# Kernel optimization log

Measured on AMD Instinct MI355X. Metric: run time of the kernel, lower is better.

## Reference

```python
import jax, jax.numpy as jnp
import numpy as np

OUT, IN, G, TOK = 4096, 4096, 16, 8192


def setup_inputs() -> dict:
    key = jax.random.key(0)
    k1, k2, k3, k4 = jax.random.split(key, 4)
    x = jax.random.normal(k1, (TOK, IN), dtype=jnp.float32)
    # packed int4 pairs: each byte holds two 4-bit values (low nibble, high nibble)
    weight_q4 = jax.random.randint(k2, (OUT * IN // G, G // 2), 0, 256, dtype=jnp.int32)
    # per-group abs-max normalization, strictly positive
    weight_norm = jax.random.uniform(k3, (OUT * IN // G, 1), dtype=jnp.float16, minval=0.01, maxval=1.0)
    bias = jax.random.normal(k4, (OUT,), dtype=jnp.float32) * 0.01
    return {"x": x, "weight_q4": weight_q4, "weight_norm": weight_norm, "bias": bias}


def _dequant_4bit(weight_q4, weight_norm):
    # unpack nibbles: even positions = low nibble, odd positions = high nibble
    low = weight_q4 & 15
    high = (weight_q4 >> 4) & 15
    q8 = jnp.stack([low, high], axis=-1).reshape(weight_q4.shape[0], -1)  # [n_groups, G]
    norm = weight_norm.astype(jnp.float32)                                 # [n_groups, 1]
    w = (q8.astype(jnp.float32) / 15.0) * 2.0 * norm - norm               # [-norm, +norm]
    return w.reshape(OUT, IN)


def reference(x, weight_q4, weight_norm, bias):
    W = _dequant_4bit(weight_q4, weight_norm)  # [OUT, IN] fp32
    return x @ W.T + bias                      # [TOK, OUT]
```

## Files before the change

### kernel.cpp

```cpp
#include <hip/hip_runtime.h>
#include <hip/hip_fp16.h>

#define M_TOK 8192
#define N_OUT 4096
#define K_IN  4096
#define GRP   16

typedef __bf16 bf16x8 __attribute__((ext_vector_type(8)));
typedef float  f32x4  __attribute__((ext_vector_type(4)));
typedef unsigned short ushort8 __attribute__((ext_vector_type(8)));

__device__ __forceinline__ float bfbits(unsigned short h) {
    unsigned int u = ((unsigned int)h) << 16;
    return __builtin_bit_cast(float, u);
}

#define GLDS16(gp, sp) __builtin_amdgcn_global_load_lds(                      \
        (const __attribute__((address_space(1))) void*)(gp),                  \
        (__attribute__((address_space(3))) void*)(sp), 16, 0, 0)

__device__ __forceinline__ void detect_block(const void* __restrict__ xv,
                                             const void* __restrict__ nrmv,
                                             const void* __restrict__ biasv,
                                             int* s_modes) {
    const int tid = threadIdx.x;
    if (tid < 64) {
        const unsigned short* px = (const unsigned short*)xv;
        unsigned short hx = px[tid * 2];
        int ex = (hx >> 7) & 0xFF;
        bool xok = ((ex >= 64 && ex <= 134) || (hx & 0x7FFF) == 0);
        unsigned long long xb = __ballot(xok);

        const unsigned short* pn = (const unsigned short*)nrmv;
        unsigned short hn = pn[tid & 31];
        float v16 = __half2float(__builtin_bit_cast(__half, hn));
        float vbf = bfbits(hn);
        unsigned long long b16 = __ballot(v16 > 0.0085f && v16 < 1.02f);
        unsigned long long bbf = __ballot(vbf > 0.0085f && vbf < 1.02f);

        const unsigned short* pb = (const unsigned short*)biasv;
        unsigned short hb = pb[tid * 2];
        int eb = (hb >> 7) & 0xFF;
        bool bok = ((eb >= 64 && eb <= 134) || (hb & 0x7FFF) == 0);
        unsigned long long bb = __ballot(bok);

        if (tid == 0) {
            s_modes[0] = (xb == ~0ULL) ? 1 : 0;
            s_modes[1] = (b16 == ~0ULL) ? 0 : ((bbf == ~0ULL) ? 1 : 2);
            s_modes[2] = (bb == ~0ULL) ? 1 : 0;
        }
    }
    __syncthreads();
}

__global__ __launch_bounds__(256) void prep_all(const void* __restrict__ xv,
                                                const int* __restrict__ q4,
                                                const void* __restrict__ nrmv,
                                                const void* __restrict__ biasv,
                                                __bf16* __restrict__ W,
                                                __bf16* __restrict__ X) {
    __shared__ int s_modes[3];
    detect_block(xv, nrmv, biasv, s_modes);
    const int tid = threadIdx.x;

    if (blockIdx.x < 4096) {
        const int nmode = s_modes[1];
        const int t = blockIdx.x * 256 + tid;
        const int4* qp = (const int4*)q4 + (size_t)t * 2;
        int4 a4 = qp[0], c4 = qp[1];
        float nm;
        if (nmode == 0)      nm = __half2float(((const __half*)nrmv)[t]);
        else if (nmode == 1) nm = bfbits(((const unsigned short*)nrmv)[t]);
        else                 nm = ((const float*)nrmv)[t];
        float s = nm * (2.0f / 15.0f);
        int qs[8] = {a4.x, a4.y, a4.z, a4.w, c4.x, c4.y, c4.z, c4.w};
        bf16x8 v0, v1;
#pragma unroll
        for (int u = 0; u < 8; ++u) {
            float lo = fmaf((float)(qs[u] & 15), s, -nm);
            float hi = fmaf((float)((qs[u] >> 4) & 15), s, -nm);
            if (u < 4) { v0[2 * u] = (__bf16)lo; v0[2 * u + 1] = (__bf16)hi; }
            else       { v1[2 * (u - 4)] = (__bf16)lo; v1[2 * (u - 4) + 1] = (__bf16)hi; }
        }
        bf16x8* wp = (bf16x8*)(W + (size_t)t * 16);
        wp[0] = v0; wp[1] = v1;
    } else {
        if (s_modes[0] == 1) return;
        const int bx = blockIdx.x - 4096;
        const int total8 = M_TOK * K_IN / 8;
        const int stride = 2048 * 256;
        for (int i = bx * 256 + tid; i < total8; i += stride) {
            const float4* fp = (const float4*)xv + (size_t)i * 2;
            float4 f0 = fp[0], f1 = fp[1];
            bf16x8 u;
            u[0] = (__bf16)f0.x; u[1] = (__bf16)f0.y; u[2] = (__bf16)f0.z; u[3] = (__bf16)f0.w;
            u[4] = (__bf16)f1.x; u[5] = (__bf16)f1.y; u[6] = (__bf16)f1.z; u[7] = (__bf16)f1.w;
            *(bf16x8*)(X + (size_t)i * 8) = u;
        }
    }
}

__global__ __launch_bounds__(256, 3) void gemm_glds(
        const void* __restrict__ xv, const __bf16* __restrict__ Xws,
        const __bf16* __restrict__ W, const void* __restrict__ nrmv,
        const void* __restrict__ biasv, float* __restrict__ out) {
    __shared__ __align__(16) __bf16 As[128 * 32];
    __shared__ __align__(16) __bf16 Bs[128 * 32];
    __shared__ int s_modes[3];

    detect_block(xv, nrmv, biasv, s_modes);
    const int xmode = s_modes[0];
    const int bmode = s_modes[2];
    const __bf16* A = xmode ? (const __bf16*)xv : Xws;

    const int bid = ((blockIdx.x & 7) << 8) + (blockIdx.x >> 3);
    const int n0 = (bid & 31) * 128;
    const int m0 = (bid >> 5) * 128;

    const int tid = threadIdx.x;
    const int w  = tid >> 6;
    const int l  = tid & 63;
    const int r  = l & 15;
    const int q  = l >> 4;
    const int wm = (w >> 1) * 64;
    const int wn = (w & 1) * 64;

    const int c0 = w * 2;
    const int lr = l >> 2;
    const int lc = (l & 3) * 8;
    const __bf16* ga0 = A + (size_t)(m0 + c0 * 16 + lr) * K_IN + lc;
    const __bf16* gb0 = W + (size_t)(n0 + c0 * 16 + lr) * K_IN + lc;
    __bf16* la0 = As + c0 * 512;
    __bf16* lb0 = Bs + c0 * 512;

    f32x4 acc[4][4];
#pragma unroll
    for (int j = 0; j < 4; ++j) {
        const int bidx = n0 + wn + j * 16 + r;
        float bv = (bmode == 0) ? ((const float*)biasv)[bidx]
                                : bfbits(((const unsigned short*)biasv)[bidx]);
#pragma unroll
        for (int i = 0; i < 4; ++i) {
            acc[i][j][0] = bv; acc[i][j][1] = bv; acc[i][j][2] = bv; acc[i][j][3] = bv;
        }
    }

    for (int k0 = 0; k0 < K_IN; k0 += 32) {
        __syncthreads();
        GLDS16(ga0 + k0,                      la0);
        GLDS16(ga0 + k0 + (size_t)16 * K_IN,  la0 + 512);
        GLDS16(gb0 + k0,                      lb0);
        GLDS16(gb0 + k0 + (size_t)16 * K_IN,  lb0 + 512);
        __syncthreads();

        bf16x8 af[4], bf[4];
#pragma unroll
        for (int i = 0; i < 4; ++i)
            af[i] = *(const bf16x8*)(As + (wm + i * 16 + r) * 32 + q * 8);
#pragma unroll
        for (int j = 0; j < 4; ++j)
            bf[j] = *(const bf16x8*)(Bs + (wn + j * 16 + r) * 32 + q * 8);

#pragma unroll
        for (int i = 0; i < 4; ++i)
#pragma unroll
            for (int j = 0; j < 4; ++j)
                acc[i][j] = __builtin_amdgcn_mfma_f32_16x16x32_bf16(
                    af[i], bf[j], acc[i][j], 0, 0, 0);
    }

#pragma unroll
    for (int i = 0; i < 4; ++i) {
        const int row = m0 + wm + i * 16 + q * 4;
#pragma unroll
        for (int j = 0; j < 4; ++j) {
            const int col = n0 + wn + j * 16 + r;
            float* p = out + (size_t)row * N_OUT + col;
            p[0 * N_OUT] = acc[i][j][0];
            p[1 * N_OUT] = acc[i][j][1];
            p[2 * N_OUT] = acc[i][j][2];
            p[3 * N_OUT] = acc[i][j][3];
        }
    }
}

__global__ __launch_bounds__(256, 2) void gemm_fused(
        const void* __restrict__ xv,
        const int* __restrict__ q4, const void* __restrict__ nrmv,
        const void* __restrict__ biasv, float* __restrict__ out) {
    __shared__ __align__(16) __bf16 As[128 * 32];
    __shared__ __align__(16) __bf16 Bs[128 * 32];
    __shared__ int s_modes[3];

    detect_block(xv, nrmv, biasv, s_modes);
    const int tid = threadIdx.x;
    const int xmode = s_modes[0];
    const int nmode = s_modes[1];
    const int bmode = s_modes[2];

    const int bid = blockIdx.x;
    const int n0 = (bid & 31) * 128;
    const int m0 = (bid >> 5) * 128;

    const int w  = tid >> 6;
    const int l  = tid & 63;
    const int r  = l & 15;
    const int q  = l >> 4;
    const int wm = (w >> 1) * 64;
    const int wn = (w & 1) * 64;

    const int arow = tid >> 1;
    const int acol = (tid & 1) * 16;
    const size_t aoff = (size_t)(m0 + arow) * K_IN + acol;

    const int brow = tid >> 1;
    const int bgc  = tid & 1;

    f32x4 acc[4][4];
#pragma unroll
    for (int j = 0; j < 4; ++j) {
        const int bidx = n0 + wn + j * 16 + r;
        float bv = (bmode == 0) ? ((const float*)biasv)[bidx]
                                : bfbits(((const unsigned short*)biasv)[bidx]);
#pragma unroll
        for (int i = 0; i < 4; ++i) {
            acc[i][j][0] = bv; acc[i][j][1] = bv; acc[i][j][2] = bv; acc[i][j][3] = bv;
        }
    }

    for (int k0 = 0; k0 < K_IN; k0 += 32) {
        __syncthreads();
        {
            const int g = (n0 + brow) * (K_IN / GRP) + (k0 >> 4) + bgc;
            const int4* qp = (const int4*)q4 + (size_t)g * 2;
            int4 a4 = qp[0], c4 = qp[1];
            float nm;
            if (nmode == 0)      nm = __half2float(((const __half*)nrmv)[g]);
            else if (nmode == 1) nm = bfbits(((const unsigned short*)nrmv)[g]);
            else                 nm = ((const float*)nrmv)[g];
            float s = nm * (2.0f / 15.0f);
            int qs[8] = {a4.x, a4.y, a4.z, a4.w, c4.x, c4.y, c4.z, c4.w};
            bf16x8 v0, v1;
#pragma unroll
            for (int u = 0; u < 8; ++u) {
                float lo = fmaf((float)(qs[u] & 15), s, -nm);
                float hi = fmaf((float)((qs[u] >> 4) & 15), s, -nm);
                if (u < 4) { v0[2 * u] = (__bf16)lo; v0[2 * u + 1] = (__bf16)hi; }
                else       { v1[2 * (u - 4)] = (__bf16)lo; v1[2 * (u - 4) + 1] = (__bf16)hi; }
            }
            bf16x8* bp = (bf16x8*)(Bs + brow * 32 + bgc * 16);
            bp[0] = v0; bp[1] = v1;
        }

        if (xmode == 0) {
            const float4* ap = (const float4*)((const float*)xv + aoff + k0);
            float4 f0 = ap[0], f1 = ap[1], f2 = ap[2], f3 = ap[3];
            bf16x8 u0, u1;
            u0[0] = (__bf16)f0.x; u0[1] = (__bf16)f0.y; u0[2] = (__bf16)f0.z; u0[3] = (__bf16)f0.w;
            u0[4] = (__bf16)f1.x; u0[5] = (__bf16)f1.y; u0[6] = (__bf16)f1.z; u0[7] = (__bf16)f1.w;
            u1[0] = (__bf16)f2.x; u1[1] = (__bf16)f2.y; u1[2] = (__bf16)f2.z; u1[3] = (__bf16)f2.w;
            u1[4] = (__bf16)f3.x; u1[5] = (__bf16)f3.y; u1[6] = (__bf16)f3.z; u1[7] = (__bf16)f3.w;
            bf16x8* asp = (bf16x8*)(As + arow * 32 + acol);
            asp[0] = u0; asp[1] = u1;
        } else {
            const ushort8* ap = (const ushort8*)((const unsigned short*)xv + aoff + k0);
            ushort8 u0 = ap[0], u1 = ap[1];
            bf16x8* asp = (bf16x8*)(As + arow * 32 + acol);
            asp[0] = __builtin_bit_cast(bf16x8, u0);
            asp[1] = __builtin_bit_cast(bf16x8, u1);
        }

        __syncthreads();

        bf16x8 af[4], bf[4];
#pragma unroll
        for (int i = 0; i < 4; ++i)
            af[i] = *(const bf16x8*)(As + (wm + i * 16 + r) * 32 + q * 8);
#pragma unroll
        for (int j = 0; j < 4; ++j)
            bf[j] = *(const bf16x8*)(Bs + (wn + j * 16 + r) * 32 + q * 8);

#pragma unroll
        for (int i = 0; i < 4; ++i)
#pragma unroll
            for (int j = 0; j < 4; ++j)
                acc[i][j] = __builtin_amdgcn_mfma_f32_16x16x32_bf16(
                    af[i], bf[j], acc[i][j], 0, 0, 0);
    }

#pragma unroll
    for (int i = 0; i < 4; ++i) {
        const int row = m0 + wm + i * 16 + q * 4;
#pragma unroll
        for (int j = 0; j < 4; ++j) {
            const int col = n0 + wn + j * 16 + r;
            float* p = out + (size_t)row * N_OUT + col;
            p[0 * N_OUT] = acc[i][j][0];
            p[1 * N_OUT] = acc[i][j][1];
            p[2 * N_OUT] = acc[i][j][2];
            p[3 * N_OUT] = acc[i][j][3];
        }
    }
}

extern "C" void kernel_launch(void* const* d_in, const int* in_sizes, int n_in,
                              void* d_out, int out_size, void* d_ws, size_t ws_size,
                              hipStream_t stream) {
    const void* x    = d_in[0];
    const int*  q4   = (const int*)d_in[1];
    const void* nrm  = d_in[2];
    const void* bias = d_in[3];
    float*      out  = (float*)d_out;

    const size_t X_OFF = (size_t)N_OUT * K_IN * 2;
    const size_t NEED  = X_OFF + (size_t)M_TOK * K_IN * 2;

    if (ws_size >= NEED) {
        __bf16* W = (__bf16*)d_ws;
        __bf16* X = (__bf16*)((char*)d_ws + X_OFF);

        prep_all<<<4096 + 2048, 256, 0, stream>>>(x, q4, nrm, bias, W, X);
        gemm_glds<<<(M_TOK / 128) * (N_OUT / 128), 256, 0, stream>>>(
            x, X, W, nrm, bias, out);
    } else {
        gemm_fused<<<(M_TOK / 128) * (N_OUT / 128), 256, 0, stream>>>(
            x, q4, nrm, bias, out);
    }
}
```

Before: 582.2 us.

## Rewrite GEMM with 256x256 tiles, triple-buffered LDS and swizzled layout

Replaces the 128x128 single-buffer GEMM with a 512-thread, 256x256-tile kernel. It stages tiles three deep through global-to-LDS loads, waiting with vmcnt so the loads for tile t+2 overlap compute on tile t. It also XOR-swizzles the LDS columns to avoid bank conflicts and raises wave priority around the MFMA block. The larger tiles and the pipeline aim to cut global traffic per flop and hide load latency. The cost is 96KB of LDS and 128 accumulator registers per thread, which lowers occupancy, and the grid shrinks to 512 blocks with the grouped block ordering dropped.

```diff
diff --git a/kernel.cpp b/kernel.cpp
--- a/kernel.cpp
+++ b/kernel.cpp
@@ -100,12 +100,12 @@
     }
 }
 
-__global__ __launch_bounds__(256, 3) void gemm_glds(
+__global__ __launch_bounds__(512, 2) void gemm256(
         const void* __restrict__ xv, const __bf16* __restrict__ Xws,
         const __bf16* __restrict__ W, const void* __restrict__ nrmv,
         const void* __restrict__ biasv, float* __restrict__ out) {
-    __shared__ __align__(16) __bf16 As[128 * 32];
-    __shared__ __align__(16) __bf16 Bs[128 * 32];
+    __shared__ __align__(16) __bf16 As3[3 * 8192];
+    __shared__ __align__(16) __bf16 Bs3[3 * 8192];
     __shared__ int s_modes[3];
 
     detect_block(xv, nrmv, biasv, s_modes);
@@ -113,64 +113,95 @@
     const int bmode = s_modes[2];
     const __bf16* A = xmode ? (const __bf16*)xv : Xws;
 
-    const int bid = ((blockIdx.x & 7) << 8) + (blockIdx.x >> 3);
-    const int n0 = (bid & 31) * 128;
-    const int m0 = (bid >> 5) * 128;
+    const int bid = blockIdx.x;
+    const int n0 = (bid & 15) * 256;
+    const int m0 = (bid >> 4) * 256;
 
     const int tid = threadIdx.x;
     const int w  = tid >> 6;
     const int l  = tid & 63;
     const int r  = l & 15;
     const int q  = l >> 4;
-    const int wm = (w >> 1) * 64;
-    const int wn = (w & 1) * 64;
-
-    const int c0 = w * 2;
-    const int lr = l >> 2;
-    const int lc = (l & 3) * 8;
-    const __bf16* ga0 = A + (size_t)(m0 + c0 * 16 + lr) * K_IN + lc;
-    const __bf16* gb0 = W + (size_t)(n0 + c0 * 16 + lr) * K_IN + lc;
-    __bf16* la0 = As + c0 * 512;
-    __bf16* lb0 = Bs + c0 * 512;
-
-    f32x4 acc[4][4];
+    const int wm = (w >> 2) * 128;
+    const int wn = (w & 3) * 64;
+    const int xq8 = (q ^ (r & 3)) * 8;
+
+    const int rr    = w * 16 + (l >> 2);
+    const int cperm = ((l & 3) ^ ((l >> 2) & 3)) * 8;
+    const __bf16* gA = A + (size_t)(m0 + rr) * K_IN + cperm;
+    const __bf16* gB = W + (size_t)(n0 + rr) * K_IN + cperm;
+    __bf16* laB = As3 + w * 512;
+    __bf16* lbB = Bs3 + w * 512;
+
+    auto stage = [&](int t, int b) {
+        const __bf16* at = gA + t * 32;
+        const __bf16* bt = gB + t * 32;
+        __bf16* la = laB + b * 8192;
+        __bf16* lb = lbB + b * 8192;
+        GLDS16(at,                       la);
+        GLDS16(at + (size_t)128 * K_IN,  la + 4096);
+        GLDS16(bt,                       lb);
+        GLDS16(bt + (size_t)128 * K_IN,  lb + 4096);
+    };
+
+    f32x4 acc[8][4];
 #pragma unroll
     for (int j = 0; j < 4; ++j) {
         const int bidx = n0 + wn + j * 16 + r;
         float bv = (bmode == 0) ? ((const float*)biasv)[bidx]
                                 : bfbits(((const unsigned short*)biasv)[bidx]);
 #pragma unroll
-        for (int i = 0; i < 4; ++i) {
+        for (int i = 0; i < 8; ++i) {
             acc[i][j][0] = bv; acc[i][j][1] = bv; acc[i][j][2] = bv; acc[i][j][3] = bv;
         }
     }
 
-    for (int k0 = 0; k0 < K_IN; k0 += 32) {
-        __syncthreads();
-        GLDS16(ga0 + k0,                      la0);
-        GLDS16(ga0 + k0 + (size_t)16 * K_IN,  la0 + 512);
-        GLDS16(gb0 + k0,                      lb0);
-        GLDS16(gb0 + k0 + (size_t)16 * K_IN,  lb0 + 512);
-        __syncthreads();
-
-        bf16x8 af[4], bf[4];
-#pragma unroll
-        for (int i = 0; i < 4; ++i)
-            af[i] = *(const bf16x8*)(As + (wm + i * 16 + r) * 32 + q * 8);
+    auto compute = [&](int b) {
+        const __bf16* Ab = As3 + b * 8192;
+        const __bf16* Bb = Bs3 + b * 8192;
+        bf16x8 af[8], bfr[4];
+#pragma unroll
+        for (int i = 0; i < 8; ++i)
+            af[i] = *(const bf16x8*)(Ab + (wm + i * 16 + r) * 32 + xq8);
 #pragma unroll
         for (int j = 0; j < 4; ++j)
-            bf[j] = *(const bf16x8*)(Bs + (wn + j * 16 + r) * 32 + q * 8);
-
-#pragma unroll
-        for (int i = 0; i < 4; ++i)
+            bfr[j] = *(const bf16x8*)(Bb + (wn + j * 16 + r) * 32 + xq8);
+        __builtin_amdgcn_s_setprio(1);
+#pragma unroll
+        for (int i = 0; i < 8; ++i)
 #pragma unroll
             for (int j = 0; j < 4; ++j)
                 acc[i][j] = __builtin_amdgcn_mfma_f32_16x16x32_bf16(
-                    af[i], bf[j], acc[i][j], 0, 0, 0);
-    }
-
-#pragma unroll
-    for (int i = 0; i < 4; ++i) {
+                    af[i], bfr[j], acc[i][j], 0, 0, 0);
+        __builtin_amdgcn_s_setprio(0);
+    };
+
+    const int NT = K_IN / 32;
+
+    stage(0, 0);
+    stage(1, 1);
+    asm volatile("s_waitcnt vmcnt(4)" ::: "memory");
+    __builtin_amdgcn_s_barrier();
+
+    int bc = 0, bs = 2;
+    for (int t = 0; t < NT - 2; ++t) {
+        stage(t + 2, bs);
+        compute(bc);
+        __builtin_amdgcn_sched_barrier(0);
+        asm volatile("s_waitcnt vmcnt(4)" ::: "memory");
+        __builtin_amdgcn_s_barrier();
+        bc = (bc == 2) ? 0 : bc + 1;
+        bs = (bs == 2) ? 0 : bs + 1;
+    }
+    compute(bc);
+    __builtin_amdgcn_sched_barrier(0);
+    asm volatile("s_waitcnt vmcnt(0)" ::: "memory");
+    __builtin_amdgcn_s_barrier();
+    bc = (bc == 2) ? 0 : bc + 1;
+    compute(bc);
+
+#pragma unroll
+    for (int i = 0; i < 8; ++i) {
         const int row = m0 + wm + i * 16 + q * 4;
 #pragma unroll
         for (int j = 0; j < 4; ++j) {
@@ -320,7 +351,7 @@
         __bf16* X = (__bf16*)((char*)d_ws + X_OFF);
 
         prep_all<<<4096 + 2048, 256, 0, stream>>>(x, q4, nrm, bias, W, X);
-        gemm_glds<<<(M_TOK / 128) * (N_OUT / 128), 256, 0, stream>>>(
+        gemm256<<<(M_TOK / 256) * (N_OUT / 256), 512, 0, stream>>>(
             x, X, W, nrm, bias, out);
     } else {
         gemm_fused<<<(M_TOK / 128) * (N_OUT / 128), 256, 0, stream>>>(
```

New measurement: 570.6 us. -2.0%, faster.

## Replace 128x128 GEMM with 256x256 eight-phase double-buffered pipelined kernel

Applied to the files above, without the earlier changes.

Replaces the simple single-buffered 128x128 tile bf16 GEMM with a 512-thread, 256x256-tile kernel that uses a K-tile of 64, double-buffered LDS, and an eight-phase schedule. Each phase interleaves global-to-LDS loads for future tiles with MFMA work, using explicit waitcnt, barriers and setprio. It also adds an XOR swizzle on LDS columns to reduce bank conflicts, and drops the block remapping. The aim is to hide global load latency and raise arithmetic intensity per block, at the cost of 128 KB of LDS, one block per CU, and a fragile hand-tuned synchronisation scheme.

```diff
diff --git a/kernel.cpp b/kernel.cpp
--- a/kernel.cpp
+++ b/kernel.cpp
@@ -100,12 +100,48 @@
     }
 }
 
-__global__ __launch_bounds__(256, 3) void gemm_glds(
+#define PHASE(d, h, p, WT, ...) do {                                          \
+    const __bf16* Ar_ = As + (d)*16384 + aregion;                             \
+    const __bf16* Br_ = Bs + (d)*16384 + bregion;                             \
+    bf16x8 af_[4][2], bv_[2][2];                                              \
+    _Pragma("unroll")                                                         \
+    for (int ii = 0; ii < 4; ++ii) {                                          \
+        const int R_ = (((h)*4 + ii)*16 + r) * 64;                            \
+        af_[ii][0] = *(const bf16x8*)(Ar_ + R_ + qs8);                        \
+        af_[ii][1] = *(const bf16x8*)(Ar_ + R_ + 32 + qs8);                   \
+    }                                                                         \
+    _Pragma("unroll")                                                         \
+    for (int jj = 0; jj < 2; ++jj) {                                          \
+        const int RB_ = (brow0 + ((p)*2 + jj)*16 + r) * 64;                   \
+        bv_[jj][0] = *(const bf16x8*)(Br_ + RB_ + qs8);                       \
+        bv_[jj][1] = *(const bf16x8*)(Br_ + RB_ + 32 + qs8);                  \
+    }                                                                         \
+    __VA_ARGS__                                                               \
+    if ((WT) == 2) asm volatile("s_waitcnt vmcnt(2)" ::: "memory");           \
+    if ((WT) == 1) asm volatile("s_waitcnt vmcnt(0)" ::: "memory");           \
+    __builtin_amdgcn_s_barrier();                                             \
+    asm volatile("s_waitcnt lgkmcnt(0)" ::: "memory");                        \
+    __builtin_amdgcn_sched_barrier(0);                                        \
+    __builtin_amdgcn_s_setprio(1);                                            \
+    _Pragma("unroll")                                                         \
+    for (int ii = 0; ii < 4; ++ii)                                            \
+    _Pragma("unroll")                                                         \
+    for (int jj = 0; jj < 2; ++jj) {                                          \
+        acc[(h)*4+ii][(p)*2+jj] = __builtin_amdgcn_mfma_f32_16x16x32_bf16(    \
+            af_[ii][0], bv_[jj][0], acc[(h)*4+ii][(p)*2+jj], 0, 0, 0);        \
+        acc[(h)*4+ii][(p)*2+jj] = __builtin_amdgcn_mfma_f32_16x16x32_bf16(    \
+            af_[ii][1], bv_[jj][1], acc[(h)*4+ii][(p)*2+jj], 0, 0, 0);        \
+    }                                                                         \
+    __builtin_amdgcn_s_setprio(0);                                            \
+    __builtin_amdgcn_s_barrier();                                             \
+} while (0)
+
+__global__ __launch_bounds__(512, 1) void gemm8ph(
         const void* __restrict__ xv, const __bf16* __restrict__ Xws,
         const __bf16* __restrict__ W, const void* __restrict__ nrmv,
         const void* __restrict__ biasv, float* __restrict__ out) {
-    __shared__ __align__(16) __bf16 As[128 * 32];
-    __shared__ __align__(16) __bf16 Bs[128 * 32];
+    __shared__ __align__(16) __bf16 As[2 * 16384];
+    __shared__ __align__(16) __bf16 Bs[2 * 16384];
     __shared__ int s_modes[3];
 
     detect_block(xv, nrmv, biasv, s_modes);
@@ -113,64 +149,73 @@
     const int bmode = s_modes[2];
     const __bf16* A = xmode ? (const __bf16*)xv : Xws;
 
-    const int bid = ((blockIdx.x & 7) << 8) + (blockIdx.x >> 3);
-    const int n0 = (bid & 31) * 128;
-    const int m0 = (bid >> 5) * 128;
+    const int bid = blockIdx.x;
+    const int n0 = (bid & 15) * 256;
+    const int m0 = (bid >> 4) * 256;
 
     const int tid = threadIdx.x;
     const int w  = tid >> 6;
     const int l  = tid & 63;
     const int r  = l & 15;
     const int q  = l >> 4;
-    const int wm = (w >> 1) * 64;
-    const int wn = (w & 1) * 64;
-
-    const int c0 = w * 2;
-    const int lr = l >> 2;
-    const int lc = (l & 3) * 8;
-    const __bf16* ga0 = A + (size_t)(m0 + c0 * 16 + lr) * K_IN + lc;
-    const __bf16* gb0 = W + (size_t)(n0 + c0 * 16 + lr) * K_IN + lc;
-    __bf16* la0 = As + c0 * 512;
-    __bf16* lb0 = Bs + c0 * 512;
-
-    f32x4 acc[4][4];
+    const int wm = (w >> 2) * 128;
+    const int wn = (w & 3) * 64;
+    const int qs8 = (q ^ (((r >> 2) & 1) << 1)) * 8;
+    const int aregion = (w >> 2) * 8192;
+    const int bregion = ((w & 3) >> 1) * 8192;
+    const int brow0   = (w & 1) * 64;
+
+    const int srow = tid >> 3;
+    const int scol = ((tid & 7) ^ (((tid >> 5) & 1) << 1)) * 8;
+    const __bf16* gA = A + (size_t)(m0 + srow) * K_IN + scol;
+    const __bf16* gB = W + (size_t)(n0 + srow) * K_IN + scol;
+
+    auto stgA = [&](int d, int hi, int kt) {
+        const size_t ko = (size_t)kt * 64;
+        GLDS16(gA + (size_t)(hi * 64) * K_IN + ko,       As + d * 16384 + hi * 4096 + tid * 8);
+        GLDS16(gA + (size_t)(hi * 64 + 128) * K_IN + ko, As + d * 16384 + 8192 + hi * 4096 + tid * 8);
+    };
+    auto stgB = [&](int d, int hi, int kt) {
+        const size_t ko = (size_t)kt * 64;
+        GLDS16(gB + (size_t)(hi * 128) * K_IN + ko,      Bs + d * 16384 + hi * 8192 + tid * 8);
+        GLDS16(gB + (size_t)(hi * 128 + 64) * K_IN + ko, Bs + d * 16384 + hi * 8192 + 4096 + tid * 8);
+    };
+
+    f32x4 acc[8][4];
 #pragma unroll
     for (int j = 0; j < 4; ++j) {
         const int bidx = n0 + wn + j * 16 + r;
         float bv = (bmode == 0) ? ((const float*)biasv)[bidx]
                                 : bfbits(((const unsigned short*)biasv)[bidx]);
 #pragma unroll
-        for (int i = 0; i < 4; ++i) {
+        for (int i = 0; i < 8; ++i) {
             acc[i][j][0] = bv; acc[i][j][1] = bv; acc[i][j][2] = bv; acc[i][j][3] = bv;
         }
     }
 
-    for (int k0 = 0; k0 < K_IN; k0 += 32) {
-        __syncthreads();
-        GLDS16(ga0 + k0,                      la0);
-        GLDS16(ga0 + k0 + (size_t)16 * K_IN,  la0 + 512);
-        GLDS16(gb0 + k0,                      lb0);
-        GLDS16(gb0 + k0 + (size_t)16 * K_IN,  lb0 + 512);
-        __syncthreads();
-
-        bf16x8 af[4], bf[4];
-#pragma unroll
-        for (int i = 0; i < 4; ++i)
-            af[i] = *(const bf16x8*)(As + (wm + i * 16 + r) * 32 + q * 8);
-#pragma unroll
-        for (int j = 0; j < 4; ++j)
-            bf[j] = *(const bf16x8*)(Bs + (wn + j * 16 + r) * 32 + q * 8);
-
-#pragma unroll
-        for (int i = 0; i < 4; ++i)
-#pragma unroll
-            for (int j = 0; j < 4; ++j)
-                acc[i][j] = __builtin_amdgcn_mfma_f32_16x16x32_bf16(
-                    af[i], bf[j], acc[i][j], 0, 0, 0);
-    }
-
-#pragma unroll
-    for (int i = 0; i < 4; ++i) {
+    stgA(0, 0, 0); stgA(0, 1, 0); stgB(0, 0, 0); stgB(0, 1, 0);
+    stgA(1, 0, 1);
+    asm volatile("s_waitcnt vmcnt(2)" ::: "memory");
+    __builtin_amdgcn_s_barrier();
+
+    for (int i = 0; i < 32; ++i) {
+        const int k1 = 2 * i + 1, k2 = 2 * i + 2, k3 = 2 * i + 3;
+        const bool st = (i < 31);
+        const int wt4 = st ? 2 : 1;
+        const int wt8 = st ? 2 : 0;
+
+        PHASE(0, 0, 0, 0, stgA(1, 1, k1); );
+        PHASE(0, 0, 1, 0, stgB(1, 0, k1); );
+        PHASE(0, 1, 0, 0, stgB(1, 1, k1); );
+        PHASE(0, 1, 1, wt4, if (st) stgA(0, 0, k2); );
+        PHASE(1, 0, 0, 0, if (st) stgA(0, 1, k2); );
+        PHASE(1, 0, 1, 0, if (st) stgB(0, 0, k2); );
+        PHASE(1, 1, 0, 0, if (st) stgB(0, 1, k2); );
+        PHASE(1, 1, 1, wt8, if (st) stgA(1, 0, k3); );
+    }
+
+#pragma unroll
+    for (int i = 0; i < 8; ++i) {
         const int row = m0 + wm + i * 16 + q * 4;
 #pragma unroll
         for (int j = 0; j < 4; ++j) {
@@ -320,7 +365,7 @@
         __bf16* X = (__bf16*)((char*)d_ws + X_OFF);
 
         prep_all<<<4096 + 2048, 256, 0, stream>>>(x, q4, nrm, bias, W, X);
-        gemm_glds<<<(M_TOK / 128) * (N_OUT / 128), 256, 0, stream>>>(
+        gemm8ph<<<(M_TOK / 256) * (N_OUT / 256), 512, 0, stream>>>(
             x, X, W, nrm, bias, out);
     } else {
         gemm_fused<<<(M_TOK / 128) * (N_OUT / 128), 256, 0, stream>>>(
```

Measured after the change: 578.8 us. About the same (-0.6%).
